# Optimization experiments

Hardware: AMD Instinct MI355X
Metric: run time of the kernel (lower is better)

The kernel has to match this reference:

```python
import jax, jax.numpy as jnp
import numpy as np

NS = 50000   # source nodes
NT = 50000   # target nodes
E = 500000   # edges per relation
H = 128      # hidden_channels
SF, TF, ED, OUT = 64, 48, 32, 2


def setup_inputs() -> dict:
    key = jax.random.key(0)
    ks = jax.random.split(key, 40)
    n = lambda i, shape, s=1.0: jax.random.normal(ks[i], shape, jnp.float32) * s
    W = 0.05  # weight scale
    inp = {
        'x_source': n(0, (NS, SF)),
        'x_target': n(1, (NT, TF)),
        'edge_attr_st': n(2, (E, ED)),
        'enc_s_w1': n(3, (H, SF), W), 'enc_s_b1': n(4, (H,), W),
        'enc_s_w2': n(5, (H, H), W), 'enc_s_b2': n(6, (H,), W),
        'enc_t_w1': n(7, (H, TF), W), 'enc_t_b1': n(8, (H,), W),
        'enc_t_w2': n(9, (H, H), W), 'enc_t_b2': n(10, (H,), W),
        'conv_wl': n(11, (3, 4, H, H), W),
        'conv_bl': n(12, (3, 4, H), W),
        'conv_wr': n(13, (3, 4, H, H), W),
        'gate_w1': n(14, (H, 2 * H), W), 'gate_b1': n(15, (H,), W),
        'gate_w2': n(16, (1, H), W), 'gate_b2': n(17, (1,), W),
        'mlp_w1': n(18, (H, H + ED), W), 'mlp_b1': n(19, (H,), W),
        'mlp_w2': n(20, (H // 2, H), W), 'mlp_b2': n(21, (H // 2,), W),
        'mlp_w3': n(22, (OUT, H // 2), W), 'mlp_b3': n(23, (OUT,), W),
        'ei_ss': jax.random.randint(ks[24], (2, E), 0, NS),
        'ei_tt': jax.random.randint(ks[25], (2, E), 0, NT),
        'ei_st': jax.random.randint(ks[26], (2, E), 0, NS),  # row<NS, col<NT (equal here)
        'ei_ts': jax.random.randint(ks[27], (2, E), 0, NT),
    }
    return inp


def _sage(x_src, x_dst, ei, wl, bl, wr, n_dst):
    # PyG SAGEConv(mean): lin_l(scatter_mean(x_src[row] -> col)) + lin_r(x_dst)
    row, col = ei[0], ei[1]
    msg = x_src[row]                                            # [E, H]
    s = jax.ops.segment_sum(msg, col, num_segments=n_dst)      # [n_dst, H]
    cnt = jax.ops.segment_sum(jnp.ones((ei.shape[1],), x_src.dtype), col,
                              num_segments=n_dst)
    agg = s / jnp.maximum(cnt, 1.0)[:, None]
    return agg @ wl.T + bl + x_dst @ wr.T


def reference(x_source, x_target, edge_attr_st,
              enc_s_w1, enc_s_b1, enc_s_w2, enc_s_b2,
              enc_t_w1, enc_t_b1, enc_t_w2, enc_t_b2,
              conv_wl, conv_bl, conv_wr,
              gate_w1, gate_b1, gate_w2, gate_b2,
              mlp_w1, mlp_b1, mlp_w2, mlp_b2, mlp_w3, mlp_b3,
              ei_ss, ei_tt, ei_st, ei_ts):
    relu = jax.nn.relu
    # node encoders (dropout is identity in eval)
    xs = relu(x_source @ enc_s_w1.T + enc_s_b1) @ enc_s_w2.T + enc_s_b2
    xt = relu(x_target @ enc_t_w1.T + enc_t_b1) @ enc_t_w2.T + enc_t_b2

    def hetero_layer(hs, ht, l):
        # relation order: 0=ss, 1=tt, 2=st, 3=ts
        o_ss = _sage(hs, hs, ei_ss, conv_wl[l, 0], conv_bl[l, 0], conv_wr[l, 0], NS)
        o_tt = _sage(ht, ht, ei_tt, conv_wl[l, 1], conv_bl[l, 1], conv_wr[l, 1], NT)
        o_st = _sage(hs, ht, ei_st, conv_wl[l, 2], conv_bl[l, 2], conv_wr[l, 2], NT)
        o_ts = _sage(ht, hs, ei_ts, conv_wl[l, 3], conv_bl[l, 3], conv_wr[l, 3], NS)
        # HeteroConv aggr='mean' over relations per destination node type
        return (o_ss + o_ts) * 0.5, (o_tt + o_st) * 0.5

    h1s, h1t = hetero_layer(xs, xt, 0)
    h1s, h1t = relu(h1s), relu(h1t)
    h2s, h2t = hetero_layer(h1s, h1t, 1)
    h2s, h2t = relu(h2s + h1s), relu(h2t + h1t)
    h3s, h3t = hetero_layer(h2s, h2t, 2)
    h3s, h3t = relu(h3s + h2s), relu(h3t + h2t)

    # edge head on ('source','to','target') — first non-empty relation
    row, col = ei_st[0], ei_st[1]
    src_h = h3s[row]                                            # [E, H]
    tgt_h = h3t[col]                                            # [E, H]
    cat = jnp.concatenate([src_h, tgt_h], axis=1)               # [E, 2H]
    gate = jax.nn.sigmoid(relu(cat @ gate_w1.T + gate_b1) @ gate_w2.T + gate_b2)
    combined = src_h * gate + tgt_h * (1.0 - gate)
    feat = jnp.concatenate([combined, edge_attr_st], axis=1)    # [E, H+ED]
    h = relu(feat @ mlp_w1.T + mlp_b1)
    h = relu(h @ mlp_w2.T + mlp_b2)
    return h @ mlp_w3.T + mlp_b3                                # [E, OUT]
```

## Files before the change

### kernel.cpp

```cpp
#include <hip/hip_runtime.h>
#include <cmath>

#define NSN 50000
#define NTN 50000
#define EE  500000
#define NBE ((size_t)NSN * 128)
#define NPASS 4
#define PRNG 12500

using short8 = __attribute__((ext_vector_type(8))) short;
using f32x4  = __attribute__((ext_vector_type(4))) float;
#define MFMA16(a, b, c) __builtin_amdgcn_mfma_f32_16x16x32_bf16(a, b, c, 0, 0, 0)

__device__ __forceinline__ float  b2f(ushort u) { return __uint_as_float(((uint)u) << 16); }
__device__ __forceinline__ ushort f2b(float f) {
  uint x = __float_as_uint(f);
  uint r = x + 0x7FFFu + ((x >> 16) & 1u);
  return (ushort)(r >> 16);
}
__device__ __forceinline__ float blo(uint x) { return __uint_as_float(x << 16); }
__device__ __forceinline__ float bhi(uint x) { return __uint_as_float(x & 0xFFFF0000u); }
__device__ __forceinline__ uint  pk2(float a, float b) { return (uint)f2b(a) | ((uint)f2b(b) << 16); }

__global__ void cvtall_k(const float* __restrict__ xs, const float* __restrict__ xt,
                         const float* __restrict__ wl,
                         const float* __restrict__ esw1, const float* __restrict__ esw2,
                         const float* __restrict__ etw1, const float* __restrict__ etw2,
                         ushort* __restrict__ xsB, ushort* __restrict__ xtB,
                         ushort* __restrict__ wlB, ushort* __restrict__ esw1B,
                         ushort* __restrict__ esw2B, ushort* __restrict__ etw1B,
                         ushort* __restrict__ etw2B) {
  int i = blockIdx.x * 256 + threadIdx.x;
  if (i < 3200000) { xsB[i] = f2b(xs[i]); return; }
  i -= 3200000;
  if (i < 3200000) {
    int r = i >> 6, k = i & 63;
    xtB[i] = (k < 48) ? f2b(xt[(size_t)r * 48 + k]) : (ushort)0;
    return;
  }
  i -= 3200000;
  if (i < 196608) { wlB[i] = f2b(wl[i]); return; }
  i -= 196608;
  if (i < 8192) { esw1B[i] = f2b(esw1[i]); return; }
  i -= 8192;
  if (i < 16384) { esw2B[i] = f2b(esw2[i]); return; }
  i -= 16384;
  if (i < 8192) {
    int r = i >> 6, k = i & 63;
    etw1B[i] = (k < 48) ? f2b(etw1[(size_t)r * 48 + k]) : (ushort)0;
    return;
  }
  i -= 8192;
  if (i < 16384) { etw2B[i] = f2b(etw2[i]); return; }
}

__global__ void wrc_k(const float* __restrict__ wr, const float* __restrict__ bl,
                      ushort* __restrict__ wrcB, float* __restrict__ blc) {
  int z = blockIdx.y;
  int l = z >> 1, dd = z & 1;
  int r1 = dd ? 1 : 0, r2 = dd ? 2 : 3;
  int idx = blockIdx.x * 256 + threadIdx.x;
  if (idx < 16384) {
    wrcB[(size_t)z * 16384 + idx] =
        f2b(wr[(size_t)(l * 4 + r1) * 16384 + idx] + wr[(size_t)(l * 4 + r2) * 16384 + idx]);
    if (idx < 128)
      blc[z * 128 + idx] = bl[(l * 4 + r1) * 128 + idx] + bl[(l * 4 + r2) * 128 + idx];
  }
}

__global__ void headw_k(const float* __restrict__ gw1, const float* __restrict__ mw1,
                        const float* __restrict__ mw2, const float* __restrict__ gb1,
                        const float* __restrict__ mb1,
                        ushort* __restrict__ Whead, float* __restrict__ biasHead,
                        ushort* __restrict__ w1eB, ushort* __restrict__ w2B) {
  int idx = blockIdx.x * 256 + threadIdx.x;
  if (idx < 65536) {
    int z = idx >> 15, rr = (idx >> 7) & 255, c = idx & 127;
    float v = (rr < 128) ? gw1[(size_t)rr * 256 + z * 128 + c]
                         : mw1[(size_t)(rr - 128) * 160 + c];
    Whead[idx] = f2b(v);
  } else if (idx < 69632) {
    int i = idx - 65536;
    w1eB[i] = f2b(mw1[(size_t)(i >> 5) * 160 + 128 + (i & 31)]);
  } else if (idx < 77824) {
    int i = idx - 69632;
    w2B[i] = f2b(mw2[i]);
  } else if (idx < 78336) {
    int i = idx - 77824;
    int z = i >> 8, n = i & 255;
    biasHead[i] = (n < 128) ? (z ? 0.f : gb1[n]) : mb1[n - 128];
  }
}

__global__ void count4_k(const int* __restrict__ e0, const int* __restrict__ e1,
                         const int* __restrict__ e2, const int* __restrict__ e3,
                         int* __restrict__ cnt) {
  int rel = blockIdx.y;
  const int* col = (rel == 0 ? e0 : rel == 1 ? e1 : rel == 2 ? e2 : e3) + EE;
  int i = blockIdx.x * 256 + threadIdx.x;
  if (i < EE) atomicAdd(&cnt[rel * 50000 + col[i]], 1);
}

__global__ __launch_bounds__(256) void scanA_k(const int* __restrict__ cnt,
                                               int* __restrict__ loc,
                                               int* __restrict__ bsum) {
  __shared__ int ws[4];
  int rel = blockIdx.y, b = blockIdx.x, t = threadIdx.x;
  const int* c = cnt + (size_t)rel * 50000;
  int base = b * 2048 + t * 8;
  int v[8], s = 0;
  #pragma unroll
  for (int i = 0; i < 8; ++i) {
    int idx = base + i;
    v[i] = (idx < 50000) ? c[idx] : 0;
    s += v[i];
  }
  int lane = t & 63, w = t >> 6;
  int x = s;
  #pragma unroll
  for (int d = 1; d < 64; d <<= 1) {
    int y = __shfl_up(x, d, 64);
    if (lane >= d) x += y;
  }
  if (lane == 63) ws[w] = x;
  __syncthreads();
  int add = 0;
  for (int ww = 0; ww < w; ++ww) add += ws[ww];
  int run = add + x - s;
  #pragma unroll
  for (int i = 0; i < 8; ++i) {
    int idx = base + i;
    run += v[i];
    if (idx < 50000) loc[(size_t)rel * 50000 + idx] = run;
  }
  if (t == 255) bsum[rel * 25 + b] = add + x;
}
__global__ void scanB_k(int* __restrict__ bsum) {
  int t = threadIdx.x;
  if (t < 4) {
    int s = 0;
    for (int b = 0; b < 25; ++b) {
      int v = bsum[t * 25 + b];
      bsum[t * 25 + b] = s;
      s += v;
    }
  }
}
__global__ void scanC_k(const int* __restrict__ cnt, int* __restrict__ loc,
                        const int* __restrict__ bsum, int* __restrict__ off,
                        int* __restrict__ cur) {
  int rel = blockIdx.y;
  int i = blockIdx.x * 256 + threadIdx.x;
  if (i < 50000) {
    int incl = loc[(size_t)rel * 50000 + i] + bsum[rel * 25 + i / 2048];
    off[(size_t)rel * 50001 + i + 1] = incl;
    cur[(size_t)rel * 50000 + i] = incl - cnt[(size_t)rel * 50000 + i];
    if (i == 0) off[(size_t)rel * 50001] = 0;
  }
}

__global__ void fillP_k(const int* __restrict__ e0, const int* __restrict__ e1,
                        const int* __restrict__ e2, const int* __restrict__ e3,
                        int* __restrict__ cur, int* __restrict__ adj, int pass) {
  int rel = blockIdx.y;
  const int* ei = rel == 0 ? e0 : rel == 1 ? e1 : rel == 2 ? e2 : e3;
  int e = blockIdx.x * 256 + threadIdx.x;
  if (e < EE) {
    int c = ei[EE + e];
    if (c >= pass * PRNG && c < (pass + 1) * PRNG) {
      int pos = atomicAdd(&cur[rel * 50000 + c], 1);
      adj[(size_t)rel * EE + pos] = ei[e];
    }
  }
}

__global__ __launch_bounds__(256) void gather4_k(
    const ushort* __restrict__ hs, const ushort* __restrict__ ht,
    const int* __restrict__ off4, const int* __restrict__ adj4,
    ushort* __restrict__ m0, ushort* __restrict__ m1,
    ushort* __restrict__ m2, ushort* __restrict__ m3, int N) {
  int r = blockIdx.y;
  const ushort* src = (r == 0 || r == 2) ? hs : ht;
  ushort* dst = r == 0 ? m0 : (r == 1 ? m1 : (r == 2 ? m2 : m3));
  const int* off = off4 + r * 50001;
  const int* adj = adj4 + (size_t)r * EE;
  int t = threadIdx.x;
  int n = blockIdx.x * 4 + (t >> 6);
  if (n >= N) return;
  int lane = t & 63, g = lane >> 4, i = lane & 15;
  int s = off[n], e = off[n + 1];
  float a[8] = {};
  for (int k = s + g; k < e; k += 4) {
    int row = adj[k];
    uint4 v = *(const uint4*)(src + (size_t)row * 128 + i * 8);
    a[0] += blo(v.x); a[1] += bhi(v.x);
    a[2] += blo(v.y); a[3] += bhi(v.y);
    a[4] += blo(v.z); a[5] += bhi(v.z);
    a[6] += blo(v.w); a[7] += bhi(v.w);
  }
  #pragma unroll
  for (int c = 0; c < 8; ++c) {
    a[c] += __shfl_xor(a[c], 16, 64);
    a[c] += __shfl_xor(a[c], 32, 64);
  }
  if (g == 0) {
    float inv = 1.f / (float)max(e - s, 1);
    uint4 o;
    o.x = pk2(a[0] * inv, a[1] * inv);
    o.y = pk2(a[2] * inv, a[3] * inv);
    o.z = pk2(a[4] * inv, a[5] * inv);
    o.w = pk2(a[6] * inv, a[7] * inv);
    *(uint4*)(dst + (size_t)n * 128 + i * 8) = o;
  }
}

template <int MODE>
__device__ __forceinline__ void gemm_body(
    ushort (*As)[40], ushort (*Ws)[40],
    const ushort* __restrict__ A, const ushort* __restrict__ W,
    const float* __restrict__ bias, ushort* __restrict__ C,
    int M, int K, int ldc, int m0) {
  int t = threadIdx.x;
  int lane = t & 63, w = t >> 6, wm = w >> 1, wn = w & 1;
  f32x4 zz = {0.f, 0.f, 0.f, 0.f};
  f32x4 acc[4][4];
  #pragma unroll
  for (int i = 0; i < 4; ++i)
    #pragma unroll
    for (int j = 0; j < 4; ++j) acc[i][j] = zz;
  for (int kb = 0; kb < K; kb += 32) {
    #pragma unroll
    for (int s = 0; s < 2; ++s) {
      int idx = t + s * 256;
      int r = idx >> 2, c = idx & 3;
      int gm = m0 + r;
      uint4 va = make_uint4(0, 0, 0, 0);
      if (gm < M) va = *(const uint4*)(A + (size_t)gm * K + kb + c * 8);
      *(uint4*)&As[r][c * 8] = va;
      *(uint4*)&Ws[r][c * 8] = *(const uint4*)(W + (size_t)r * K + kb + c * 8);
    }
    __syncthreads();
    short8 af[4], bf[4];
    #pragma unroll
    for (int mf = 0; mf < 4; ++mf)
      af[mf] = *(const short8*)&As[wm * 64 + mf * 16 + (lane & 15)][(lane >> 4) * 8];
    #pragma unroll
    for (int nf = 0; nf < 4; ++nf)
      bf[nf] = *(const short8*)&Ws[wn * 64 + nf * 16 + (lane & 15)][(lane >> 4) * 8];
    #pragma unroll
    for (int mf = 0; mf < 4; ++mf)
      #pragma unroll
      for (int nf = 0; nf < 4; ++nf) acc[mf][nf] = MFMA16(af[mf], bf[nf], acc[mf][nf]);
    __syncthreads();
  }
  int r0 = (lane >> 4) * 4, nin = lane & 15;
  #pragma unroll
  for (int mf = 0; mf < 4; ++mf)
    #pragma unroll
    for (int nf = 0; nf < 4; ++nf) {
      int n = wn * 64 + nf * 16 + nin;
      float bv = bias ? bias[n] : 0.f;
      #pragma unroll
      for (int i = 0; i < 4; ++i) {
        int gm = m0 + wm * 64 + mf * 16 + r0 + i;
        if (gm >= M) continue;
        float v = acc[mf][nf][i] + bv;
        if (MODE == 1) v = fmaxf(v, 0.f);
        C[(size_t)gm * ldc + n] = f2b(v);
      }
    }
}

template <int MODE>
__global__ __launch_bounds__(256) void enc_k(
    const ushort* A0, const ushort* A1, const ushort* W0, const ushort* W1,
    const float* b0, const float* b1, ushort* C0, ushort* C1, int M, int K) {
  __shared__ alignas(16) ushort As[128][40];
  __shared__ alignas(16) ushort Ws[128][40];
  int y = blockIdx.y;
  gemm_body<MODE>(As, Ws, y ? A1 : A0, y ? W1 : W0, y ? b1 : b0, y ? C1 : C0,
                  M, K, 128, blockIdx.x * 128);
}

__global__ __launch_bounds__(256) void gemmH_k(
    const ushort* Abase, const ushort* Whead, const float* biasHead,
    ushort* pS, ushort* pT) {
  __shared__ alignas(16) ushort As[128][40];
  __shared__ alignas(16) ushort Ws[128][40];
  int z = blockIdx.z, ny = blockIdx.y;
  gemm_body<0>(As, Ws, Abase + (size_t)z * NBE,
               Whead + ((size_t)z * 256 + ny * 128) * 128,
               biasHead + z * 256 + ny * 128,
               (z ? pT : pS) + ny * 128,
               NSN, 128, 256, blockIdx.x * 128);
}

template <int RES>
__global__ __launch_bounds__(256) void lgemm_k(
    const ushort* __restrict__ hs, const ushort* __restrict__ ht,
    const ushort* __restrict__ m0, const ushort* __restrict__ m1,
    const ushort* __restrict__ m2, const ushort* __restrict__ m3,
    const ushort* __restrict__ wlL, const ushort* __restrict__ wrcL,
    const float* __restrict__ blcL,
    ushort* __restrict__ hsOut, ushort* __restrict__ htOut, int M) {
  __shared__ alignas(16) ushort As[128][40];
  __shared__ alignas(16) ushort Ws[128][40];
  int t = threadIdx.x;
  int y = blockIdx.y;
  int m0i = blockIdx.x * 128;
  const ushort* A0 = y ? m1 : m0;
  const ushort* A1 = y ? m2 : m3;
  const ushort* self = y ? ht : hs;
  const ushort* W0 = wlL + (size_t)(y ? 1 : 0) * 16384;
  const ushort* W1 = wlL + (size_t)(y ? 2 : 3) * 16384;
  const ushort* W2 = wrcL + (size_t)y * 16384;
  const float* bias = blcL + y * 128;
  ushort* C = y ? htOut : hsOut;

  int lane = t & 63, w = t >> 6, wm = w >> 1, wn = w & 1;
  f32x4 zz = {0.f, 0.f, 0.f, 0.f};
  f32x4 acc[4][4];
  #pragma unroll
  for (int i = 0; i < 4; ++i)
    #pragma unroll
    for (int j = 0; j < 4; ++j) acc[i][j] = zz;
  for (int p = 0; p < 3; ++p) {
    const ushort* A = p == 0 ? A0 : (p == 1 ? A1 : self);
    const ushort* Wp = p == 0 ? W0 : (p == 1 ? W1 : W2);
    for (int kb = 0; kb < 128; kb += 32) {
      #pragma unroll
      for (int s = 0; s < 2; ++s) {
        int idx = t + s * 256;
        int r = idx >> 2, c = idx & 3;
        int gm = m0i + r;
        uint4 va = make_uint4(0, 0, 0, 0);
        if (gm < M) va = *(const uint4*)(A + (size_t)gm * 128 + kb + c * 8);
        *(uint4*)&As[r][c * 8] = va;
        *(uint4*)&Ws[r][c * 8] = *(const uint4*)(Wp + (size_t)r * 128 + kb + c * 8);
      }
      __syncthreads();
      short8 af[4], bf[4];
      #pragma unroll
      for (int mf = 0; mf < 4; ++mf)
        af[mf] = *(const short8*)&As[wm * 64 + mf * 16 + (lane & 15)][(lane >> 4) * 8];
      #pragma unroll
      for (int nf = 0; nf < 4; ++nf)
        bf[nf] = *(const short8*)&Ws[wn * 64 + nf * 16 + (lane & 15)][(lane >> 4) * 8];
      #pragma unroll
      for (int mf = 0; mf < 4; ++mf)
        #pragma unroll
        for (int nf = 0; nf < 4; ++nf) acc[mf][nf] = MFMA16(af[mf], bf[nf], acc[mf][nf]);
      __syncthreads();
    }
  }
  int r0 = (lane >> 4) * 4, nin = lane & 15;
  #pragma unroll
  for (int mf = 0; mf < 4; ++mf)
    #pragma unroll
    for (int nf = 0; nf < 4; ++nf) {
      int n = wn * 64 + nf * 16 + nin;
      float bv = bias[n];
      #pragma unroll
      for (int i = 0; i < 4; ++i) {
        int gm = m0i + wm * 64 + mf * 16 + r0 + i;
        if (gm >= M) continue;
        float v = 0.5f * (acc[mf][nf][i] + bv);
        if (RES) v += b2f(self[(size_t)gm * 128 + n]);
        C[(size_t)gm * 128 + n] = f2b(fmaxf(v, 0.f));
      }
    }
}

__global__ __launch_bounds__(256) void head_k(
    const ushort* __restrict__ pS, const ushort* __restrict__ pT,
    const int* __restrict__ ei, const float* __restrict__ ea,
    const ushort* __restrict__ w1eB, const ushort* __restrict__ w2B,
    const float* __restrict__ gw2, const float* __restrict__ gb2p,
    const float* __restrict__ mb2, const float* __restrict__ mw3,
    const float* __restrict__ mb3, float* __restrict__ out, int E) {
  __shared__ alignas(16) ushort h1s[64][136];
  __shared__ int er[64], ec[64];
  __shared__ alignas(16) float gw2s[128];
  __shared__ alignas(16) float mw3s[128];
  __shared__ float mb2s[64];
  float (*h2F)[68] = (float(*)[68])&h1s[0][0];

  int t = threadIdx.x;
  int e0 = blockIdx.x * 64;
  if (t < 64) {
    int eg = e0 + t;
    er[t] = (eg < E) ? ei[eg] : 0;
    mb2s[t] = mb2[t];
  } else if (t < 128) {
    int q = t - 64;
    int eg = e0 + q;
    ec[q] = (eg < E) ? ei[E + eg] : 0;
  }
  if (t < 128) gw2s[t] = gw2[t];
  else mw3s[t - 128] = mw3[t - 128];
  __syncthreads();
  int lane = t & 63, w = t >> 6;
  {
    int erow = e0 + w * 16 + (lane & 15);
    float4 f0 = make_float4(0, 0, 0, 0), f1 = make_float4(0, 0, 0, 0);
    if (erow < E) {
      f0 = *(const float4*)(ea + (size_t)erow * 32 + (lane >> 4) * 8);
      f1 = *(const float4*)(ea + (size_t)erow * 32 + (lane >> 4) * 8 + 4);
    }
    union { short8 s; uint4 u; } cv;
    cv.u = make_uint4(pk2(f0.x, f0.y), pk2(f0.z, f0.w), pk2(f1.x, f1.y), pk2(f1.z, f1.w));
    short8 a = cv.s;
    int ebase = w * 16 + (lane >> 4) * 4;
    #pragma unroll
    for (int nf = 0; nf < 8; ++nf) {
      short8 b = *(const short8*)(w1eB + (size_t)(nf * 16 + (lane & 15)) * 32 + (lane >> 4) * 8);
      f32x4 cz = {0.f, 0.f, 0.f, 0.f};
      cz = MFMA16(a, b, cz);
      int jj = nf * 16 + (lane & 15);
      #pragma unroll
      for (int i = 0; i < 4; ++i) h1s[ebase + i][jj] = f2b(cz[i]);
    }
  }
  __syncthreads();
  {
    int el = lane >> 2, q = lane & 3, e = w * 16 + el;
    int j0 = q * 32;
    const ushort* ps = pS + (size_t)er[e] * 256;
    const ushort* pt = pT + (size_t)ec[e] * 256;
    float dot = 0.f;
    #pragma unroll
    for (int cc = 0; cc < 4; ++cc) {
      int j = j0 + cc * 8;
      uint4 ga = *(const uint4*)(ps + j);
      uint4 gb = *(const uint4*)(pt + j);
      const float* gp = &gw2s[j];
      float h;
      h = fmaxf(blo(ga.x) + blo(gb.x), 0.f); dot = fmaf(h, gp[0], dot);
      h = fmaxf(bhi(ga.x) + bhi(gb.x), 0.f); dot = fmaf(h, gp[1], dot);
      h = fmaxf(blo(ga.y) + blo(gb.y), 0.f); dot = fmaf(h, gp[2], dot);
      h = fmaxf(bhi(ga.y) + bhi(gb.y), 0.f); dot = fmaf(h, gp[3], dot);
      h = fmaxf(blo(ga.z) + blo(gb.z), 0.f); dot = fmaf(h, gp[4], dot);
      h = fmaxf(bhi(ga.z) + bhi(gb.z), 0.f); dot = fmaf(h, gp[5], dot);
      h = fmaxf(blo(ga.w) + blo(gb.w), 0.f); dot = fmaf(h, gp[6], dot);
      h = fmaxf(bhi(ga.w) + bhi(gb.w), 0.f); dot = fmaf(h, gp[7], dot);
    }
    dot += __shfl_xor(dot, 1, 64);
    dot += __shfl_xor(dot, 2, 64);
    float g = 1.f / (1.f + __expf(-(dot + gb2p[0])));
    float om = 1.f - g;
    #pragma unroll
    for (int cc = 0; cc < 4; ++cc) {
      int j = j0 + cc * 8;
      uint4 uu = *(const uint4*)(ps + 128 + j);
      uint4 vv = *(const uint4*)(pt + 128 + j);
      uint4 ee = *(const uint4*)&h1s[e][j];
      uint o0 = pk2(fmaxf(fmaf(g, blo(uu.x), om * blo(vv.x)) + blo(ee.x), 0.f),
                    fmaxf(fmaf(g, bhi(uu.x), om * bhi(vv.x)) + bhi(ee.x), 0.f));
      uint o1 = pk2(fmaxf(fmaf(g, blo(uu.y), om * blo(vv.y)) + blo(ee.y), 0.f),
                    fmaxf(fmaf(g, bhi(uu.y), om * bhi(vv.y)) + bhi(ee.y), 0.f));
      uint o2 = pk2(fmaxf(fmaf(g, blo(uu.z), om * blo(vv.z)) + blo(ee.z), 0.f),
                    fmaxf(fmaf(g, bhi(uu.z), om * bhi(vv.z)) + bhi(ee.z), 0.f));
      uint o3 = pk2(fmaxf(fmaf(g, blo(uu.w), om * blo(vv.w)) + blo(ee.w), 0.f),
                    fmaxf(fmaf(g, bhi(uu.w), om * bhi(vv.w)) + bhi(ee.w), 0.f));
      *(uint4*)&h1s[e][j] = make_uint4(o0, o1, o2, o3);
    }
  }
  __syncthreads();
  {
    f32x4 zz = {0.f, 0.f, 0.f, 0.f};
    f32x4 acc[4] = {zz, zz, zz, zz};
    #pragma unroll
    for (int ks = 0; ks < 4; ++ks) {
      short8 a = *(const short8*)&h1s[w * 16 + (lane & 15)][ks * 32 + (lane >> 4) * 8];
      #pragma unroll
      for (int nf = 0; nf < 4; ++nf) {
        short8 b = *(const short8*)(w2B + (size_t)(nf * 16 + (lane & 15)) * 128 + ks * 32 + (lane >> 4) * 8);
        acc[nf] = MFMA16(a, b, acc[nf]);
      }
    }
    __syncthreads();
    int ebase = w * 16 + (lane >> 4) * 4;
    #pragma unroll
    for (int nf = 0; nf < 4; ++nf) {
      int n = nf * 16 + (lane & 15);
      #pragma unroll
      for (int i = 0; i < 4; ++i)
        h2F[ebase + i][n] = fmaxf(acc[nf][i] + mb2s[n], 0.f);
    }
  }
  __syncthreads();
  if (t < 128) {
    int e = t >> 1, o = t & 1;
    int eg = e0 + e;
    if (eg < E) {
      float s = mb3[o];
      #pragma unroll
      for (int kk = 0; kk < 64; kk += 4) {
        float4 hv = *(const float4*)&h2F[e][kk];
        float4 wv = *(const float4*)&mw3s[o * 64 + kk];
        s = fmaf(hv.x, wv.x, s); s = fmaf(hv.y, wv.y, s);
        s = fmaf(hv.z, wv.z, s); s = fmaf(hv.w, wv.w, s);
      }
      out[(size_t)eg * 2 + o] = s;
    }
  }
}

extern "C" void kernel_launch(void* const* d_in, const int* in_sizes, int n_in,
                              void* d_out, int out_size, void* d_ws, size_t ws_size,
                              hipStream_t stream) {
  const float* x_source = (const float*)d_in[0];
  const float* x_target = (const float*)d_in[1];
  const float* edge_attr = (const float*)d_in[2];
  const float* enc_s_w1 = (const float*)d_in[3];
  const float* enc_s_b1 = (const float*)d_in[4];
  const float* enc_s_w2 = (const float*)d_in[5];
  const float* enc_s_b2 = (const float*)d_in[6];
  const float* enc_t_w1 = (const float*)d_in[7];
  const float* enc_t_b1 = (const float*)d_in[8];
  const float* enc_t_w2 = (const float*)d_in[9];
  const float* enc_t_b2 = (const float*)d_in[10];
  const float* conv_wl = (const float*)d_in[11];
  const float* conv_bl = (const float*)d_in[12];
  const float* conv_wr = (const float*)d_in[13];
  const float* gate_w1 = (const float*)d_in[14];
  const float* gate_b1 = (const float*)d_in[15];
  const float* gate_w2 = (const float*)d_in[16];
  const float* gate_b2 = (const float*)d_in[17];
  const float* mlp_w1 = (const float*)d_in[18];
  const float* mlp_b1 = (const float*)d_in[19];
  const float* mlp_w2 = (const float*)d_in[20];
  const float* mlp_b2 = (const float*)d_in[21];
  const float* mlp_w3 = (const float*)d_in[22];
  const float* mlp_b3 = (const float*)d_in[23];
  const int* ei[4] = {(const int*)d_in[24], (const int*)d_in[25],
                      (const int*)d_in[26], (const int*)d_in[27]};
  float* out = (float*)d_out;

  char* wsp = (char*)d_ws;
  size_t off = 0;
  auto alloc = [&](size_t bytes) {
    char* p = wsp + off;
    off += (bytes + 255) & ~(size_t)255;
    return p;
  };
  ushort* nbase = (ushort*)alloc(4 * NBE * 2);
  ushort* nb[4];
  for (int i = 0; i < 4; ++i) nb[i] = nbase + (size_t)i * NBE;
  ushort* shared4 = (ushort*)alloc(4 * NBE * 2);
  ushort* mB[4];
  for (int i = 0; i < 4; ++i) mB[i] = shared4 + (size_t)i * NBE;
  int* adj4 = (int*)alloc((size_t)4 * EE * 4);
  int* off4 = (int*)alloc(4 * 50001 * 4);
  int* cur4 = (int*)alloc(4 * 50000 * 4);
  int* cnt4 = (int*)alloc(4 * 50000 * 4);
  int* bsum = (int*)alloc(128 * 4);
  ushort* xsB = (ushort*)alloc((size_t)NSN * 64 * 2);
  ushort* xtB = (ushort*)alloc((size_t)NTN * 64 * 2);
  ushort* esw1B = (ushort*)alloc(128 * 64 * 2);
  ushort* esw2B = (ushort*)alloc(128 * 128 * 2);
  ushort* etw1B = (ushort*)alloc(128 * 64 * 2);
  ushort* etw2B = (ushort*)alloc(128 * 128 * 2);
  ushort* wlB = (ushort*)alloc((size_t)12 * 16384 * 2);
  ushort* wrcB = (ushort*)alloc((size_t)6 * 16384 * 2);
  float* blc = (float*)alloc(6 * 128 * 4);
  ushort* Whead = (ushort*)alloc((size_t)2 * 256 * 128 * 2);
  float* biasHead = (float*)alloc(2 * 256 * 4);
  ushort* w1eB = (ushort*)alloc(128 * 32 * 2);
  ushort* w2B = (ushort*)alloc(64 * 128 * 2);

  hipMemsetAsync(cnt4, 0, 4 * 50000 * sizeof(int), stream);
  int cb = (EE + 255) / 256;
  count4_k<<<dim3(cb, 4), 256, 0, stream>>>(ei[0], ei[1], ei[2], ei[3], cnt4);
  scanA_k<<<dim3(25, 4), 256, 0, stream>>>(cnt4, cur4, bsum);
  scanB_k<<<1, 64, 0, stream>>>(bsum);
  scanC_k<<<dim3((50000 + 255) / 256, 4), 256, 0, stream>>>(cnt4, cur4, bsum, off4, cur4);
  for (int p = 0; p < NPASS; ++p)
    fillP_k<<<dim3(cb, 4), 256, 0, stream>>>(ei[0], ei[1], ei[2], ei[3], cur4, adj4, p);

  cvtall_k<<<(6645760 + 255) / 256, 256, 0, stream>>>(
      x_source, x_target, conv_wl, enc_s_w1, enc_s_w2, enc_t_w1, enc_t_w2,
      xsB, xtB, wlB, esw1B, esw2B, etw1B, etw2B);
  wrc_k<<<dim3(64, 6), 256, 0, stream>>>(conv_wr, conv_bl, wrcB, blc);
  headw_k<<<307, 256, 0, stream>>>(gate_w1, mlp_w1, mlp_w2, gate_b1, mlp_b1,
                                   Whead, biasHead, w1eB, w2B);

  int gm = (NSN + 127) / 128;
  enc_k<1><<<dim3(gm, 2), 256, 0, stream>>>(xsB, xtB, esw1B, etw1B,
      enc_s_b1, enc_t_b1, nb[2], nb[3], NSN, 64);
  enc_k<0><<<dim3(gm, 2), 256, 0, stream>>>(nb[2], nb[3], esw2B, etw2B,
      enc_s_b2, enc_t_b2, nb[0], nb[1], NSN, 128);

  int gb = (NSN + 3) / 4;
  {
    gather4_k<<<dim3(gb, 4), 256, 0, stream>>>(nb[0], nb[1], off4, adj4,
        mB[0], mB[1], mB[2], mB[3], NSN);
    lgemm_k<0><<<dim3(gm, 2), 256, 0, stream>>>(nb[0], nb[1],
        mB[0], mB[1], mB[2], mB[3], wlB, wrcB, blc, nb[2], nb[3], NSN);
    gather4_k<<<dim3(gb, 4), 256, 0, stream>>>(nb[2], nb[3], off4, adj4,
        mB[0], mB[1], mB[2], mB[3], NSN);
    lgemm_k<1><<<dim3(gm, 2), 256, 0, stream>>>(nb[2], nb[3],
        mB[0], mB[1], mB[2], mB[3], wlB + (size_t)4 * 16384,
        wrcB + (size_t)2 * 16384, blc + 256, nb[0], nb[1], NSN);
    gather4_k<<<dim3(gb, 4), 256, 0, stream>>>(nb[0], nb[1], off4, adj4,
        mB[0], mB[1], mB[2], mB[3], NSN);
    lgemm_k<1><<<dim3(gm, 2), 256, 0, stream>>>(nb[0], nb[1],
        mB[0], mB[1], mB[2], mB[3], wlB + (size_t)8 * 16384,
        wrcB + (size_t)4 * 16384, blc + 512, nb[2], nb[3], NSN);
  }

  ushort* pS = shared4;
  ushort* pT = shared4 + 2 * NBE;
  gemmH_k<<<dim3(gm, 2, 2), 256, 0, stream>>>(nbase + 2 * NBE, Whead, biasHead, pS, pT);

  head_k<<<(EE + 63) / 64, 256, 0, stream>>>(pS, pT, ei[2], edge_attr, w1eB, w2B,
      gate_w2, gate_b2, mlp_b2, mlp_w3, mlp_b3, out, EE);
}
```

Before: 843.4 us.

## Process head edges in column-sorted CSR order with XCD-aware block swizzle

The edge head now walks edges of the source-to-target relation in CSR order sorted by target column, using the CSR adjacency for rows, a new colOf array for columns and an adjE permutation that maps back to original edge ids. This makes the pT gathers highly local and should improve cache reuse. The block index is also swizzled so that contiguous edge ranges land on the same XCD, which keeps their L2 traffic together. The encoder launches are moved ahead of CSR construction so that xsB and xtB can be reused as scratch for adjE and colOf. In exchange, edge_attr reads and output writes become scattered, and an extra colof kernel is added.

```diff
diff --git a/kernel.cpp b/kernel.cpp
--- a/kernel.cpp
+++ b/kernel.cpp
@@ -161,7 +161,8 @@
 
 __global__ void fillP_k(const int* __restrict__ e0, const int* __restrict__ e1,
                         const int* __restrict__ e2, const int* __restrict__ e3,
-                        int* __restrict__ cur, int* __restrict__ adj, int pass) {
+                        int* __restrict__ cur, int* __restrict__ adj,
+                        int* __restrict__ adjE, int pass) {
   int rel = blockIdx.y;
   const int* ei = rel == 0 ? e0 : rel == 1 ? e1 : rel == 2 ? e2 : e3;
   int e = blockIdx.x * 256 + threadIdx.x;
@@ -170,7 +171,16 @@
     if (c >= pass * PRNG && c < (pass + 1) * PRNG) {
       int pos = atomicAdd(&cur[rel * 50000 + c], 1);
       adj[(size_t)rel * EE + pos] = ei[e];
-    }
+      if (rel == 2) adjE[pos] = e;
+    }
+  }
+}
+
+__global__ void colof_k(const int* __restrict__ off, int* __restrict__ colOf, int N) {
+  int n = blockIdx.x * 256 + threadIdx.x;
+  if (n < N) {
+    int s = off[n], e = off[n + 1];
+    for (int i = s; i < e; ++i) colOf[i] = n;
   }
 }
 
@@ -373,39 +383,46 @@
 
 __global__ __launch_bounds__(256) void head_k(
     const ushort* __restrict__ pS, const ushort* __restrict__ pT,
-    const int* __restrict__ ei, const float* __restrict__ ea,
+    const int* __restrict__ erowA, const int* __restrict__ ecolA,
+    const int* __restrict__ eidA, const float* __restrict__ ea,
     const ushort* __restrict__ w1eB, const ushort* __restrict__ w2B,
     const float* __restrict__ gw2, const float* __restrict__ gb2p,
     const float* __restrict__ mb2, const float* __restrict__ mw3,
     const float* __restrict__ mb3, float* __restrict__ out, int E) {
   __shared__ alignas(16) ushort h1s[64][136];
-  __shared__ int er[64], ec[64];
+  __shared__ int er[64], ec[64], eidS[64];
   __shared__ alignas(16) float gw2s[128];
   __shared__ alignas(16) float mw3s[128];
   __shared__ float mb2s[64];
   float (*h2F)[68] = (float(*)[68])&h1s[0][0];
 
+  int nwg = gridDim.x;
+  int bid = blockIdx.x;
+  int q = nwg >> 3, r = nwg & 7;
+  int xcd = bid & 7, sub = bid >> 3;
+  int swz = (xcd < r ? xcd * (q + 1) : r * (q + 1) + (xcd - r) * q) + sub;
+  int e0 = swz * 64;
+
   int t = threadIdx.x;
-  int e0 = blockIdx.x * 64;
   if (t < 64) {
-    int eg = e0 + t;
-    er[t] = (eg < E) ? ei[eg] : 0;
+    int p = e0 + t;
+    er[t] = (p < E) ? erowA[p] : 0;
+    eidS[t] = (p < E) ? eidA[p] : -1;
     mb2s[t] = mb2[t];
   } else if (t < 128) {
-    int q = t - 64;
-    int eg = e0 + q;
-    ec[q] = (eg < E) ? ei[E + eg] : 0;
+    int p = e0 + (t - 64);
+    ec[t - 64] = (p < E) ? ecolA[p] : 0;
   }
   if (t < 128) gw2s[t] = gw2[t];
   else mw3s[t - 128] = mw3[t - 128];
   __syncthreads();
   int lane = t & 63, w = t >> 6;
   {
-    int erow = e0 + w * 16 + (lane & 15);
+    int eid = eidS[w * 16 + (lane & 15)];
     float4 f0 = make_float4(0, 0, 0, 0), f1 = make_float4(0, 0, 0, 0);
-    if (erow < E) {
-      f0 = *(const float4*)(ea + (size_t)erow * 32 + (lane >> 4) * 8);
-      f1 = *(const float4*)(ea + (size_t)erow * 32 + (lane >> 4) * 8 + 4);
+    if (eid >= 0) {
+      f0 = *(const float4*)(ea + (size_t)eid * 32 + (lane >> 4) * 8);
+      f1 = *(const float4*)(ea + (size_t)eid * 32 + (lane >> 4) * 8 + 4);
     }
     union { short8 s; uint4 u; } cv;
     cv.u = make_uint4(pk2(f0.x, f0.y), pk2(f0.z, f0.w), pk2(f1.x, f1.y), pk2(f1.z, f1.w));
@@ -423,8 +440,8 @@
   }
   __syncthreads();
   {
-    int el = lane >> 2, q = lane & 3, e = w * 16 + el;
-    int j0 = q * 32;
+    int el = lane >> 2, qq = lane & 3, e = w * 16 + el;
+    int j0 = qq * 32;
     const ushort* ps = pS + (size_t)er[e] * 256;
     const ushort* pt = pT + (size_t)ec[e] * 256;
     float dot = 0.f;
@@ -491,8 +508,8 @@
   __syncthreads();
   if (t < 128) {
     int e = t >> 1, o = t & 1;
-    int eg = e0 + e;
-    if (eg < E) {
+    int eid = eidS[e];
+    if (eid >= 0) {
       float s = mb3[o];
       #pragma unroll
       for (int kk = 0; kk < 64; kk += 4) {
@@ -501,7 +518,7 @@
         s = fmaf(hv.x, wv.x, s); s = fmaf(hv.y, wv.y, s);
         s = fmaf(hv.z, wv.z, s); s = fmaf(hv.w, wv.w, s);
       }
-      out[(size_t)eg * 2 + o] = s;
+      out[(size_t)eid * 2 + o] = s;
     }
   }
 }
@@ -569,6 +586,20 @@
   ushort* w1eB = (ushort*)alloc(128 * 32 * 2);
   ushort* w2B = (ushort*)alloc(64 * 128 * 2);
 
+  cvtall_k<<<(6645760 + 255) / 256, 256, 0, stream>>>(
+      x_source, x_target, conv_wl, enc_s_w1, enc_s_w2, enc_t_w1, enc_t_w2,
+      xsB, xtB, wlB, esw1B, esw2B, etw1B, etw2B);
+  wrc_k<<<dim3(64, 6), 256, 0, stream>>>(conv_wr, conv_bl, wrcB, blc);
+  headw_k<<<307, 256, 0, stream>>>(gate_w1, mlp_w1, mlp_w2, gate_b1, mlp_b1,
+                                   Whead, biasHead, w1eB, w2B);
+  int gm = (NSN + 127) / 128;
+  enc_k<1><<<dim3(gm, 2), 256, 0, stream>>>(xsB, xtB, esw1B, etw1B,
+      enc_s_b1, enc_t_b1, nb[2], nb[3], NSN, 64);
+  enc_k<0><<<dim3(gm, 2), 256, 0, stream>>>(nb[2], nb[3], esw2B, etw2B,
+      enc_s_b2, enc_t_b2, nb[0], nb[1], NSN, 128);
+
+  int* adjE = (int*)xsB;
+  int* colOf = (int*)xtB;
   hipMemsetAsync(cnt4, 0, 4 * 50000 * sizeof(int), stream);
   int cb = (EE + 255) / 256;
   count4_k<<<dim3(cb, 4), 256, 0, stream>>>(ei[0], ei[1], ei[2], ei[3], cnt4);
@@ -576,20 +607,8 @@
   scanB_k<<<1, 64, 0, stream>>>(bsum);
   scanC_k<<<dim3((50000 + 255) / 256, 4), 256, 0, stream>>>(cnt4, cur4, bsum, off4, cur4);
   for (int p = 0; p < NPASS; ++p)
-    fillP_k<<<dim3(cb, 4), 256, 0, stream>>>(ei[0], ei[1], ei[2], ei[3], cur4, adj4, p);
-
-  cvtall_k<<<(6645760 + 255) / 256, 256, 0, stream>>>(
-      x_source, x_target, conv_wl, enc_s_w1, enc_s_w2, enc_t_w1, enc_t_w2,
-      xsB, xtB, wlB, esw1B, esw2B, etw1B, etw2B);
-  wrc_k<<<dim3(64, 6), 256, 0, stream>>>(conv_wr, conv_bl, wrcB, blc);
-  headw_k<<<307, 256, 0, stream>>>(gate_w1, mlp_w1, mlp_w2, gate_b1, mlp_b1,
-                                   Whead, biasHead, w1eB, w2B);
-
-  int gm = (NSN + 127) / 128;
-  enc_k<1><<<dim3(gm, 2), 256, 0, stream>>>(xsB, xtB, esw1B, etw1B,
-      enc_s_b1, enc_t_b1, nb[2], nb[3], NSN, 64);
-  enc_k<0><<<dim3(gm, 2), 256, 0, stream>>>(nb[2], nb[3], esw2B, etw2B,
-      enc_s_b2, enc_t_b2, nb[0], nb[1], NSN, 128);
+    fillP_k<<<dim3(cb, 4), 256, 0, stream>>>(ei[0], ei[1], ei[2], ei[3], cur4, adj4, adjE, p);
+  colof_k<<<(50000 + 255) / 256, 256, 0, stream>>>(off4 + 2 * 50001, colOf, NTN);
 
   int gb = (NSN + 3) / 4;
   {
@@ -613,6 +632,7 @@
   ushort* pT = shared4 + 2 * NBE;
   gemmH_k<<<dim3(gm, 2, 2), 256, 0, stream>>>(nbase + 2 * NBE, Whead, biasHead, pS, pT);
 
-  head_k<<<(EE + 63) / 64, 256, 0, stream>>>(pS, pT, ei[2], edge_attr, w1eB, w2B,
+  head_k<<<(EE + 63) / 64, 256, 0, stream>>>(pS, pT,
+      adj4 + (size_t)2 * EE, colOf, adjE, edge_attr, w1eB, w2B,
       gate_w2, gate_b2, mlp_b2, mlp_w3, mlp_b3, out, EE);
 }
```

Result: no change. 834.8 us (-1.0%).
